# Performance work log

Hardware: AMD Instinct MI355X
Metric: run time of the kernel (lower is better)

## Reference

```python
import jax, jax.numpy as jnp
import numpy as np

EMBED_DIM = 1024
NUM_HEADS = 16
HEAD_DIM = EMBED_DIM // NUM_HEADS


def setup_inputs() -> dict:
    key = jax.random.key(0)
    ks = jax.random.split(key, 11)
    B, S, D = 4, 2048, EMBED_DIM
    s = 1.0 / np.sqrt(D)
    return {
        "query": jax.random.normal(ks[0], (B, S, D), jnp.float32),
        "key": jax.random.normal(ks[1], (B, S, D), jnp.float32),
        "value": jax.random.normal(ks[2], (B, S, D), jnp.float32),
        "Wq": jax.random.normal(ks[3], (D, D), jnp.float32) * s,
        "bq": jnp.zeros((D,), jnp.float32),
        "Wk": jax.random.normal(ks[4], (D, D), jnp.float32) * s,
        "bk": jnp.zeros((D,), jnp.float32),
        "Wv": jax.random.normal(ks[5], (D, D), jnp.float32) * s,
        "bv": jnp.zeros((D,), jnp.float32),
        "Wo": jax.random.normal(ks[6], (D, D), jnp.float32) * s,
        "bo": jnp.zeros((D,), jnp.float32),
    }


def _split_heads(x):
    B, S, D = x.shape
    return x.reshape(B, S, NUM_HEADS, HEAD_DIM).transpose(0, 2, 1, 3)  # (B,H,S,hd)


def reference(query, key, value, Wq, bq, Wk, bk, Wv, bv, Wo, bo):
    q = _split_heads(query @ Wq + bq)
    k = _split_heads(key @ Wk + bk)
    v = _split_heads(value @ Wv + bv)
    # naive scaled dot-product attention: full (B,H,S,S) scores materialized
    scores = jnp.einsum("bhqd,bhkd->bhqk", q, k) / np.sqrt(HEAD_DIM).astype(np.float32)
    attn = jax.nn.softmax(scores, axis=-1)
    ctx = jnp.einsum("bhqk,bhkd->bhqd", attn, v)
    B, H, S, hd = ctx.shape
    ctx = ctx.transpose(0, 2, 1, 3).reshape(B, S, H * hd)
    return ctx @ Wo + bo
```

## Files before the change

### kernel.cpp

```cpp
#include <hip/hip_runtime.h>

typedef unsigned short u16;
typedef unsigned int u32;
typedef _Float16 f16;
typedef __attribute__((ext_vector_type(8))) _Float16 f16x8;
typedef __attribute__((ext_vector_type(4))) float f32x4;
typedef __attribute__((ext_vector_type(4))) u32 u32x4;
typedef __attribute__((ext_vector_type(2))) u32 u32x2;
typedef __attribute__((ext_vector_type(4))) u16 u16x4;

static __device__ __forceinline__ u16 f16r(float f) {
  return __builtin_bit_cast(u16, (_Float16)f);
}
static __device__ __forceinline__ u32 packh(float a, float b) {
  return __builtin_bit_cast(u32, __builtin_amdgcn_cvt_pkrtz(a, b));
}
static __device__ __forceinline__ void gload16(const u16* g, u16* l) {
  __builtin_amdgcn_global_load_lds((const __attribute__((address_space(1))) void*)g,
                                   (__attribute__((address_space(3))) void*)l, 16, 0, 0);
}
static __device__ __forceinline__ void gload16f(const float* g, float* l) {
  __builtin_amdgcn_global_load_lds((const __attribute__((address_space(1))) void*)g,
                                   (__attribute__((address_space(3))) void*)l, 16, 0, 0);
}

__global__ __launch_bounds__(256) void wtrans4_k(
    const float* __restrict__ Wq, const float* __restrict__ Wk,
    const float* __restrict__ Wv, const float* __restrict__ Wo,
    u16* __restrict__ Tq, u16* __restrict__ Tk, u16* __restrict__ Tv, u16* __restrict__ To) {
  int z = blockIdx.z;
  const float* W = z == 0 ? Wq : z == 1 ? Wk : z == 2 ? Wv : Wo;
  u16* WT = z == 0 ? Tq : z == 1 ? Tk : z == 2 ? Tv : To;
  __shared__ float tile[32][33];
  int k0 = blockIdx.x * 32, n0 = blockIdx.y * 32;
  int t = threadIdx.x;
  int r = t >> 3, c = (t & 7) * 4;
  f32x4 v = *(const f32x4*)&W[(size_t)(k0 + r) * 1024 + n0 + c];
  tile[r][c + 0] = v[0]; tile[r][c + 1] = v[1]; tile[r][c + 2] = v[2]; tile[r][c + 3] = v[3];
  __syncthreads();
  int n = n0 + (t >> 3), kbase = k0 + (t & 7) * 4;
  u16x4 o;
#pragma unroll
  for (int j = 0; j < 4; j++) o[j] = f16r(tile[(t & 7) * 4 + j][t >> 3]);
  int nt = n >> 7, row = n & 127;
  int kt = kbase >> 6, lc = (kbase >> 3) & 7, e = kbase & 7;
  int pc = lc ^ (row & 7);
  *(u16x4*)&WT[((size_t)(nt * 16 + kt) * 128 + row) * 64 + pc * 8 + e] = o;
}

__global__ __launch_bounds__(256) void gemm_qkv_k(
    const float* __restrict__ Aq, const float* __restrict__ Ak, const float* __restrict__ Av,
    const u16* __restrict__ Tq, const u16* __restrict__ Tk, const u16* __restrict__ Tv,
    const float* __restrict__ bq, const float* __restrict__ bk, const float* __restrict__ bv,
    u16* __restrict__ Qo, u16* __restrict__ Ko, u16* __restrict__ Vo, float qscale) {
  int z = blockIdx.z;
  const float* A = z == 0 ? Aq : z == 1 ? Ak : Av;
  const u16* BT = z == 0 ? Tq : z == 1 ? Tk : Tv;
  const float* bias = z == 0 ? bq : z == 1 ? bk : bv;
  u16* out = z == 0 ? Qo : z == 1 ? Ko : Vo;
  int vmode = (z == 2);
  float scale = z == 0 ? qscale : 1.0f;

  __shared__ float As[128 * 64];
  __shared__ u16 Bs[128 * 64];
  int lid = blockIdx.x;
  int xcd = lid & 7, idx = lid >> 3;
  int bx = idx & 7, by = xcd * 8 + (idx >> 3);
  int n0 = bx * 128, m0 = by * 128;
  int tid = threadIdx.x, lane = tid & 63;
  int w = tid >> 6, wr = w >> 1, wc = w & 1;
  int fq = lane & 15, fc = lane >> 4;
  f32x4 acc[4][4] = {};
  const u16* BTb = BT + (size_t)bx * 16 * 8192;
  for (int ks = 0; ks < 16; ks++) {
    int kk = ks * 64;
    __syncthreads();
#pragma unroll
    for (int i = 0; i < 8; i++) {
      int ub = w * 512 + i * 64;
      int u = ub + lane;
      int row = u >> 4, pc = u & 15;
      int koff = (pc ^ (row & 15)) << 2;
      gload16f(A + (size_t)(m0 + row) * 1024 + kk + koff, &As[ub << 2]);
    }
    const u16* Bt = BTb + (size_t)ks * 8192;
#pragma unroll
    for (int i = 0; i < 4; i++) {
      int ub = w * 256 + i * 64;
      gload16(Bt + (ub << 3) + (lane << 3), &Bs[ub << 3]);
    }
    __syncthreads();
#pragma unroll
    for (int kc = 0; kc < 2; kc++) {
      f16x8 af[4], bfv[4];
#pragma unroll
      for (int mi = 0; mi < 4; mi++) {
        int row = wr * 64 + mi * 16 + fq;
        int cA = (2 * (kc * 4 + fc)) ^ fq;
        f32x4 x0 = *(const f32x4*)&As[row * 64 + cA * 4];
        f32x4 x1 = *(const f32x4*)&As[row * 64 + (cA ^ 1) * 4];
        u32x4 pk = {packh(x0[0], x0[1]), packh(x0[2], x0[3]),
                    packh(x1[0], x1[1]), packh(x1[2], x1[3])};
        af[mi] = __builtin_bit_cast(f16x8, pk);
      }
#pragma unroll
      for (int ni = 0; ni < 4; ni++) {
        int row = wc * 64 + ni * 16 + fq;
        bfv[ni] = *(const f16x8*)&Bs[row * 64 + (((kc * 4 + fc) ^ (fq & 7)) << 3)];
      }
#pragma unroll
      for (int mi = 0; mi < 4; mi++)
#pragma unroll
        for (int ni = 0; ni < 4; ni++)
          acc[mi][ni] = __builtin_amdgcn_mfma_f32_16x16x32_f16(af[mi], bfv[ni], acc[mi][ni], 0, 0, 0);
    }
  }
#pragma unroll
  for (int mi = 0; mi < 4; mi++)
#pragma unroll
    for (int ni = 0; ni < 4; ni++) {
      int n = n0 + wc * 64 + ni * 16 + fq;
      float bs = bias[n];
      int h = n >> 6, d = n & 63;
#pragma unroll
      for (int r = 0; r < 4; r++) {
        int m = m0 + wr * 64 + mi * 16 + fc * 4 + r;
        int b = m >> 11, s = m & 2047;
        float v = (acc[mi][ni][r] + bs) * scale;
        size_t o;
        if (vmode == 0) {
          int t = s >> 4, fqo = s & 15, kco = d >> 5, fco = (d & 31) >> 3, e = d & 7;
          o = (size_t)(b * 16 + h) * 131072 + (size_t)((((t * 2 + kco) * 64) + fco * 16 + fqo) * 8 + e);
        } else {
          int kvc = s >> 5, dt = d >> 4, fqo = d & 15, fco = (s & 31) >> 3, e = s & 7;
          o = (size_t)(b * 16 + h) * 131072 + (size_t)((((kvc * 4 + dt) * 64) + fco * 16 + fqo) * 8 + e);
        }
        out[o] = f16r(v);
      }
    }
}

__global__ __launch_bounds__(256) void gemm_o_k(
    const u16* __restrict__ Ag, const u16* __restrict__ Bg,
    const float* __restrict__ bias, float* __restrict__ out) {
  __shared__ u16 SA[128 * 64];
  __shared__ u16 SB[128 * 64];
  int lid = blockIdx.x;
  int xcd = lid & 7, idx = lid >> 3;
  int bx = idx & 7, by = xcd * 8 + (idx >> 3);
  int n0 = bx * 128, m0 = by * 128;
  int tid = threadIdx.x, lane = tid & 63;
  int w = tid >> 6, wr = w >> 1, wc = w & 1;
  int fq = lane & 15, fc = lane >> 4;
  f32x4 acc[4][4] = {};
  for (int ks = 0; ks < 16; ks++) {
    __syncthreads();
    size_t at = ((size_t)by * 16 + ks) * 8192;
    size_t bt = ((size_t)bx * 16 + ks) * 8192;
#pragma unroll
    for (int i = 0; i < 4; i++) {
      int ub = w * 256 + i * 64;
      int go = (ub << 3) + (lane << 3);
      gload16(Ag + at + go, &SA[ub << 3]);
      gload16(Bg + bt + go, &SB[ub << 3]);
    }
    __syncthreads();
#pragma unroll
    for (int kc = 0; kc < 2; kc++) {
      f16x8 ah[4], bh[4];
#pragma unroll
      for (int mi = 0; mi < 4; mi++) {
        int idx2 = (wr * 64 + mi * 16 + fq) * 64 + (((kc * 4 + fc) ^ (fq & 7)) << 3);
        ah[mi] = *(const f16x8*)&SA[idx2];
      }
#pragma unroll
      for (int ni = 0; ni < 4; ni++) {
        int idx2 = (wc * 64 + ni * 16 + fq) * 64 + (((kc * 4 + fc) ^ (fq & 7)) << 3);
        bh[ni] = *(const f16x8*)&SB[idx2];
      }
#pragma unroll
      for (int mi = 0; mi < 4; mi++)
#pragma unroll
        for (int ni = 0; ni < 4; ni++)
          acc[mi][ni] = __builtin_amdgcn_mfma_f32_16x16x32_f16(ah[mi], bh[ni], acc[mi][ni], 0, 0, 0);
    }
  }
#pragma unroll
  for (int mi = 0; mi < 4; mi++)
#pragma unroll
    for (int ni = 0; ni < 4; ni++) {
      int n = n0 + wc * 64 + ni * 16 + fq;
      float bs = bias[n];
#pragma unroll
      for (int r = 0; r < 4; r++) {
        int m = m0 + wr * 64 + mi * 16 + fc * 4 + r;
        out[(size_t)m * 1024 + n] = acc[mi][ni][r] + bs;
      }
    }
}

__global__ __launch_bounds__(512) void attn_k(
    const u16* __restrict__ Q, const u16* __restrict__ Kg, const u16* __restrict__ Vg,
    u16* __restrict__ ctx) {
  int lid = blockIdx.x;
  int bh = (lid & 7) * 8 + (lid >> 6);
  int qb = (lid >> 3) & 7;
  int tid = threadIdx.x, lane = tid & 63, w = tid >> 6;
  const u16* Qf = Q + (size_t)bh * 131072;
  const u16* Kf = Kg + (size_t)bh * 131072;
  const u16* Vf = Vg + (size_t)bh * 131072;
  int fq = lane & 15, fc = lane >> 4;
  int le = lane * 8;
  int q0 = qb * 256 + w * 32;

  __shared__ u16 KL[2][4096];
  __shared__ u16 VL[2][4096];
  __shared__ u16 P[8][1152];

  f16x8 qf[2][2];
#pragma unroll
  for (int mi = 0; mi < 2; mi++)
#pragma unroll
    for (int kc = 0; kc < 2; kc++)
      qf[mi][kc] = *(const f16x8*)&Qf[((((q0 + 16 * mi) >> 4) * 2 + kc) << 9) + le];

  f32x4 O[2][4] = {};
  float lrow[2] = {0.f, 0.f};

  auto stage = [&](int tt, int bb) {
    int qo = (w & 3) * 1024;
    if (w < 4) {
      const u16* Kt = Kf + tt * 4096;
      gload16(Kt + qo + le, &KL[bb][qo]);
      gload16(Kt + qo + 512 + le, &KL[bb][qo + 512]);
    } else {
      const u16* Vt = Vf + tt * 4096;
      gload16(Vt + qo + le, &VL[bb][qo]);
      gload16(Vt + qo + 512 + le, &VL[bb][qo + 512]);
    }
  };

  stage(0, 0);
  __syncthreads();

  for (int t = 0; t < 32; t++) {
    int buf = t & 1;
    if (t < 31) stage(t + 1, buf ^ 1);

    f16x8 kf[8];
#pragma unroll
    for (int c = 0; c < 8; c++) kf[c] = *(const f16x8*)&KL[buf][c * 512 + le];

    f32x4 sc[2][4] = {};
    __builtin_amdgcn_s_setprio(1);
#pragma unroll
    for (int mi = 0; mi < 2; mi++)
#pragma unroll
      for (int sub = 0; sub < 4; sub++)
#pragma unroll
        for (int kc = 0; kc < 2; kc++)
          sc[mi][sub] = __builtin_amdgcn_mfma_f32_16x16x32_f16(kf[sub * 2 + kc], qf[mi][kc],
                                                               sc[mi][sub], 0, 0, 0);
    __builtin_amdgcn_s_setprio(0);

    f16x8 vf[8];
#pragma unroll
    for (int c = 0; c < 8; c++) vf[c] = *(const f16x8*)&VL[buf][c * 512 + le];

#pragma unroll
    for (int mi = 0; mi < 2; mi++) {
      float lloc = 0.f;
#pragma unroll
      for (int sub = 0; sub < 4; sub++) {
        float p0 = __builtin_amdgcn_exp2f(sc[mi][sub][0]);
        float p1 = __builtin_amdgcn_exp2f(sc[mi][sub][1]);
        float p2 = __builtin_amdgcn_exp2f(sc[mi][sub][2]);
        float p3 = __builtin_amdgcn_exp2f(sc[mi][sub][3]);
        lloc += (p0 + p1) + (p2 + p3);
        u32x2 pw = {packh(p0, p1), packh(p2, p3)};
        *(u32x2*)&P[w][fq * 72 + sub * 16 + fc * 4] = pw;
      }
      lloc += __shfl_xor(lloc, 16);
      lloc += __shfl_xor(lloc, 32);
      lrow[mi] += lloc;

      asm volatile("s_waitcnt lgkmcnt(0)" ::: "memory");
      __builtin_amdgcn_s_setprio(1);
#pragma unroll
      for (int ch = 0; ch < 2; ch++) {
        f16x8 pa = *(const f16x8*)&P[w][fq * 72 + ch * 32 + fc * 8];
#pragma unroll
        for (int db = 0; db < 4; db++)
          O[mi][db] = __builtin_amdgcn_mfma_f32_16x16x32_f16(pa, vf[ch * 4 + db], O[mi][db], 0, 0, 0);
      }
      __builtin_amdgcn_s_setprio(0);
    }

    __syncthreads();
  }

  int b = bh >> 4, h = bh & 15;
#pragma unroll
  for (int mi = 0; mi < 2; mi++) {
    float linv[4];
#pragma unroll
    for (int r = 0; r < 4; r++) linv[r] = 1.0f / __shfl(lrow[mi], fc * 4 + r);
#pragma unroll
    for (int db = 0; db < 4; db++)
#pragma unroll
      for (int r = 0; r < 4; r++) {
        float v = O[mi][db][r] * linv[r];
        int s = q0 + mi * 16 + fc * 4 + r;
        int mrow = s & 127, mt = b * 16 + (s >> 7);
        int lc = (db * 16 + fq) >> 3, e = fq & 7;
        int pc = lc ^ (mrow & 7);
        size_t o = ((size_t)(mt * 16 + h) * 128 + mrow) * 64 + pc * 8 + e;
        ctx[o] = f16r(v);
      }
  }
}

extern "C" void kernel_launch(void* const* d_in, const int* in_sizes, int n_in,
                              void* d_out, int out_size, void* d_ws, size_t ws_size,
                              hipStream_t stream) {
  const float* query = (const float*)d_in[0];
  const float* key   = (const float*)d_in[1];
  const float* value = (const float*)d_in[2];
  const float* Wq = (const float*)d_in[3];
  const float* bq = (const float*)d_in[4];
  const float* Wk = (const float*)d_in[5];
  const float* bk = (const float*)d_in[6];
  const float* Wv = (const float*)d_in[7];
  const float* bv = (const float*)d_in[8];
  const float* Wo = (const float*)d_in[9];
  const float* bo = (const float*)d_in[10];
  float* out = (float*)d_out;

  char* ws = (char*)d_ws;
  size_t off = 0;
  auto alloc = [&](size_t bytes) {
    char* p = ws + off;
    off += (bytes + 255) & ~(size_t)255;
    return p;
  };
  u16* WqT = (u16*)alloc(1048576 * 2);
  u16* WkT = (u16*)alloc(1048576 * 2);
  u16* WvT = (u16*)alloc(1048576 * 2);
  u16* WoT = (u16*)alloc(1048576 * 2);
  u16* Qbf = (u16*)alloc((size_t)8388608 * 2);
  u16* Kbf = (u16*)alloc((size_t)8388608 * 2);
  u16* ctx = (u16*)alloc((size_t)8388608 * 2);
  u16* Vfb = (u16*)d_out;

  const float QSCALE = 0.125f * 1.44269504f;

  wtrans4_k<<<dim3(32, 32, 4), 256, 0, stream>>>(Wq, Wk, Wv, Wo, WqT, WkT, WvT, WoT);
  gemm_qkv_k<<<dim3(512, 1, 3), 256, 0, stream>>>(query, key, value, WqT, WkT, WvT,
                                                  bq, bk, bv, Qbf, Kbf, Vfb, QSCALE);
  attn_k<<<512, 512, 0, stream>>>(Qbf, Kbf, Vfb, ctx);
  gemm_o_k<<<512, 256, 0, stream>>>(ctx, WoT, bo, out);
}
```

Baseline: 199.7 us.

## Double-buffer LDS tiles in projection GEMMs with K-32 weight tiling

Both projection GEMMs now use two LDS buffers, so the global-to-LDS loads for the next K step are issued before the MFMAs on the current step, with one barrier per iteration instead of two. The transposed weight layout switches from 64-wide to 32-wide K tiles with a matching swizzle, which keeps the QKV GEMM's doubled fp32 A buffer within the LDS budget. MFMA blocks are wrapped in s_setprio to favor math waves. The cost is twice the LDS footprint, which may reduce occupancy, and the QKV GEMM now runs 32 smaller K steps.

```diff
diff --git a/kernel.cpp b/kernel.cpp
--- a/kernel.cpp
+++ b/kernel.cpp
@@ -43,9 +43,9 @@
 #pragma unroll
   for (int j = 0; j < 4; j++) o[j] = f16r(tile[(t & 7) * 4 + j][t >> 3]);
   int nt = n >> 7, row = n & 127;
-  int kt = kbase >> 6, lc = (kbase >> 3) & 7, e = kbase & 7;
-  int pc = lc ^ (row & 7);
-  *(u16x4*)&WT[((size_t)(nt * 16 + kt) * 128 + row) * 64 + pc * 8 + e] = o;
+  int kt = kbase >> 5, lc = (kbase >> 3) & 3, e = kbase & 7;
+  int pc = lc ^ (row & 3);
+  *(u16x4*)&WT[((size_t)(nt * 32 + kt) * 128 + row) * 32 + pc * 8 + e] = o;
 }
 
 __global__ __launch_bounds__(256) void gemm_qkv_k(
@@ -61,8 +61,8 @@
   int vmode = (z == 2);
   float scale = z == 0 ? qscale : 1.0f;
 
-  __shared__ float As[128 * 64];
-  __shared__ u16 Bs[128 * 64];
+  __shared__ float As[2][128 * 32];
+  __shared__ u16 Bs[2][128 * 32];
   int lid = blockIdx.x;
   int xcd = lid & 7, idx = lid >> 3;
   int bx = idx & 7, by = xcd * 8 + (idx >> 3);
@@ -71,49 +71,53 @@
   int w = tid >> 6, wr = w >> 1, wc = w & 1;
   int fq = lane & 15, fc = lane >> 4;
   f32x4 acc[4][4] = {};
-  const u16* BTb = BT + (size_t)bx * 16 * 8192;
-  for (int ks = 0; ks < 16; ks++) {
-    int kk = ks * 64;
+  const u16* BTb = BT + (size_t)bx * 131072;
+
+  auto stage = [&](int ks, int sel) {
+    const float* Ab = A + (size_t)m0 * 1024 + ks * 32;
+#pragma unroll
+    for (int i = 0; i < 4; i++) {
+      int u = (w * 4 + i) * 64 + lane;
+      int row = u >> 3, pc = u & 7;
+      int koff = (pc ^ (row & 7)) << 2;
+      gload16f(Ab + (size_t)row * 1024 + koff, &As[sel][(w * 4 + i) * 256]);
+    }
+    const u16* Bt = BTb + ks * 4096;
+#pragma unroll
+    for (int i = 0; i < 2; i++)
+      gload16(Bt + (w * 2 + i) * 512 + lane * 8, &Bs[sel][(w * 2 + i) * 512]);
+  };
+
+  stage(0, 0);
+  __syncthreads();
+#pragma unroll 2
+  for (int ks = 0; ks < 32; ks++) {
+    int cur = ks & 1;
+    if (ks < 31) stage(ks + 1, cur ^ 1);
+    f16x8 af[4], bfv[4];
+#pragma unroll
+    for (int mi = 0; mi < 4; mi++) {
+      int row = wr * 64 + mi * 16 + fq;
+      int pc0 = (2 * fc) ^ (row & 7);
+      f32x4 x0 = *(const f32x4*)&As[cur][row * 32 + pc0 * 4];
+      f32x4 x1 = *(const f32x4*)&As[cur][row * 32 + (pc0 ^ 1) * 4];
+      u32x4 pk = {packh(x0[0], x0[1]), packh(x0[2], x0[3]),
+                  packh(x1[0], x1[1]), packh(x1[2], x1[3])};
+      af[mi] = __builtin_bit_cast(f16x8, pk);
+    }
+#pragma unroll
+    for (int ni = 0; ni < 4; ni++) {
+      int row = wc * 64 + ni * 16 + fq;
+      bfv[ni] = *(const f16x8*)&Bs[cur][row * 32 + (fc ^ (row & 3)) * 8];
+    }
+    __builtin_amdgcn_s_setprio(1);
+#pragma unroll
+    for (int mi = 0; mi < 4; mi++)
+#pragma unroll
+      for (int ni = 0; ni < 4; ni++)
+        acc[mi][ni] = __builtin_amdgcn_mfma_f32_16x16x32_f16(af[mi], bfv[ni], acc[mi][ni], 0, 0, 0);
+    __builtin_amdgcn_s_setprio(0);
     __syncthreads();
-#pragma unroll
-    for (int i = 0; i < 8; i++) {
-      int ub = w * 512 + i * 64;
-      int u = ub + lane;
-      int row = u >> 4, pc = u & 15;
-      int koff = (pc ^ (row & 15)) << 2;
-      gload16f(A + (size_t)(m0 + row) * 1024 + kk + koff, &As[ub << 2]);
-    }
-    const u16* Bt = BTb + (size_t)ks * 8192;
-#pragma unroll
-    for (int i = 0; i < 4; i++) {
-      int ub = w * 256 + i * 64;
-      gload16(Bt + (ub << 3) + (lane << 3), &Bs[ub << 3]);
-    }
-    __syncthreads();
-#pragma unroll
-    for (int kc = 0; kc < 2; kc++) {
-      f16x8 af[4], bfv[4];
-#pragma unroll
-      for (int mi = 0; mi < 4; mi++) {
-        int row = wr * 64 + mi * 16 + fq;
-        int cA = (2 * (kc * 4 + fc)) ^ fq;
-        f32x4 x0 = *(const f32x4*)&As[row * 64 + cA * 4];
-        f32x4 x1 = *(const f32x4*)&As[row * 64 + (cA ^ 1) * 4];
-        u32x4 pk = {packh(x0[0], x0[1]), packh(x0[2], x0[3]),
-                    packh(x1[0], x1[1]), packh(x1[2], x1[3])};
-        af[mi] = __builtin_bit_cast(f16x8, pk);
-      }
-#pragma unroll
-      for (int ni = 0; ni < 4; ni++) {
-        int row = wc * 64 + ni * 16 + fq;
-        bfv[ni] = *(const f16x8*)&Bs[row * 64 + (((kc * 4 + fc) ^ (fq & 7)) << 3)];
-      }
-#pragma unroll
-      for (int mi = 0; mi < 4; mi++)
-#pragma unroll
-        for (int ni = 0; ni < 4; ni++)
-          acc[mi][ni] = __builtin_amdgcn_mfma_f32_16x16x32_f16(af[mi], bfv[ni], acc[mi][ni], 0, 0, 0);
-    }
   }
 #pragma unroll
   for (int mi = 0; mi < 4; mi++)
@@ -143,8 +147,8 @@
 __global__ __launch_bounds__(256) void gemm_o_k(
     const u16* __restrict__ Ag, const u16* __restrict__ Bg,
     const float* __restrict__ bias, float* __restrict__ out) {
-  __shared__ u16 SA[128 * 64];
-  __shared__ u16 SB[128 * 64];
+  __shared__ u16 SA[2][8192];
+  __shared__ u16 SB[2][8192];
   int lid = blockIdx.x;
   int xcd = lid & 7, idx = lid >> 3;
   int bx = idx & 7, by = xcd * 8 + (idx >> 3);
@@ -153,37 +157,46 @@
   int w = tid >> 6, wr = w >> 1, wc = w & 1;
   int fq = lane & 15, fc = lane >> 4;
   f32x4 acc[4][4] = {};
+
+  auto stage = [&](int ks, int sel) {
+    size_t at = ((size_t)by * 16 + ks) * 8192;
+    size_t bt = ((size_t)bx * 32 + ks * 2) * 4096;
+#pragma unroll
+    for (int i = 0; i < 4; i++) {
+      int ub = (w * 4 + i) * 512;
+      gload16(Ag + at + ub + lane * 8, &SA[sel][ub]);
+      gload16(Bg + bt + ub + lane * 8, &SB[sel][ub]);
+    }
+  };
+
+  stage(0, 0);
+  __syncthreads();
+#pragma unroll 2
   for (int ks = 0; ks < 16; ks++) {
-    __syncthreads();
-    size_t at = ((size_t)by * 16 + ks) * 8192;
-    size_t bt = ((size_t)bx * 16 + ks) * 8192;
-#pragma unroll
-    for (int i = 0; i < 4; i++) {
-      int ub = w * 256 + i * 64;
-      int go = (ub << 3) + (lane << 3);
-      gload16(Ag + at + go, &SA[ub << 3]);
-      gload16(Bg + bt + go, &SB[ub << 3]);
-    }
-    __syncthreads();
+    int cur = ks & 1;
+    if (ks < 15) stage(ks + 1, cur ^ 1);
 #pragma unroll
     for (int kc = 0; kc < 2; kc++) {
       f16x8 ah[4], bh[4];
 #pragma unroll
       for (int mi = 0; mi < 4; mi++) {
-        int idx2 = (wr * 64 + mi * 16 + fq) * 64 + (((kc * 4 + fc) ^ (fq & 7)) << 3);
-        ah[mi] = *(const f16x8*)&SA[idx2];
+        int row = wr * 64 + mi * 16 + fq;
+        ah[mi] = *(const f16x8*)&SA[cur][row * 64 + (((kc * 4 + fc) ^ (row & 7)) << 3)];
       }
 #pragma unroll
       for (int ni = 0; ni < 4; ni++) {
-        int idx2 = (wc * 64 + ni * 16 + fq) * 64 + (((kc * 4 + fc) ^ (fq & 7)) << 3);
-        bh[ni] = *(const f16x8*)&SB[idx2];
-      }
+        int row = wc * 64 + ni * 16 + fq;
+        bh[ni] = *(const f16x8*)&SB[cur][kc * 4096 + row * 32 + (fc ^ (row & 3)) * 8];
+      }
+      __builtin_amdgcn_s_setprio(1);
 #pragma unroll
       for (int mi = 0; mi < 4; mi++)
 #pragma unroll
         for (int ni = 0; ni < 4; ni++)
           acc[mi][ni] = __builtin_amdgcn_mfma_f32_16x16x32_f16(ah[mi], bh[ni], acc[mi][ni], 0, 0, 0);
-    }
+      __builtin_amdgcn_s_setprio(0);
+    }
+    __syncthreads();
   }
 #pragma unroll
   for (int mi = 0; mi < 4; mi++)
```

Result: faster. 194.0 us (-2.9%).
